# Kernel optimization log

Hardware: AMD Instinct MI355X
Metric: run time of the kernel (lower is better)

The kernel has to match this reference:

```python
import jax, jax.numpy as jnp
import numpy as np

B, L, H, R = 8, 128, 768, 24


def setup_inputs() -> dict:
    key = jax.random.key(0)
    ks = jax.random.split(key, 12)
    s = 0.02  # init scale
    f32 = jnp.float32
    inp = {
        "embed_tokens": jax.random.normal(ks[0], (B, L, H), f32),
        "attention_mask": jnp.ones((B, L), f32),
        "target_rel": jax.random.randint(ks[1], (B,), 0, R),
        # relation-judgement head
        "W_hr": jax.random.normal(ks[2], (H, H // 2), f32) * s,
        "b_hr": jnp.zeros((H // 2,), f32),
        "W_rj": jax.random.normal(ks[3], (H // 2, R), f32) * s,
        "b_rj": jnp.zeros((R,), f32),
        # relation embedding
        "rel_emb": jax.random.normal(ks[4], (R, H), f32) * s,
        # correspondence matrix head (input is concat -> 2H)
        "W_corr": jax.random.normal(ks[5], (2 * H, H), f32) * s,
        "b_corr": jnp.zeros((H,), f32),
        "W_gc": jax.random.normal(ks[6], (H, 1), f32) * s,
        "b_gc": jnp.zeros((1,), f32),
        # subject tagging head (fusion_type='concat' -> 2H in, H hidden)
        "W_sh": jax.random.normal(ks[7], (2 * H, H), f32) * s,
        "b_sh": jnp.zeros((H,), f32),
        "W_st": jax.random.normal(ks[8], (H, 3), f32) * s,
        "b_st": jnp.zeros((3,), f32),
        # object tagging head
        "W_oh": jax.random.normal(ks[9], (2 * H, H), f32) * s,
        "b_oh": jnp.zeros((H,), f32),
        "W_ot": jax.random.normal(ks[10], (H, 3), f32) * s,
        "b_ot": jnp.zeros((3,), f32),
    }
    return inp


def reference(embed_tokens, attention_mask, target_rel,
              W_hr, b_hr, W_rj, b_rj, rel_emb,
              W_corr, b_corr, W_gc, b_gc,
              W_sh, b_sh, W_st, b_st,
              W_oh, b_oh, W_ot, b_ot):
    # ---- stage 1: masked mean-pool + relation judgement (dropout = identity at inference)
    masked = embed_tokens * attention_mask[:, :, None]            # [B,L,H]
    pool = jnp.sum(masked, axis=1) / jnp.sum(attention_mask, axis=1)[:, None]  # [B,H]
    rel_hidden = jax.nn.relu(pool @ W_hr + b_hr)                  # [B,H/2]
    stage1 = rel_hidden @ W_rj + b_rj                             # [B,R]

    # ---- correspondence matrix: concat[b,i,j] = [embed[b,j], embed[b,i]]
    # Decompose concat-linear: concat @ W_corr = embed_j @ W1 + embed_i @ W2
    W1, W2 = W_corr[:H_dim(embed_tokens)], W_corr[H_dim(embed_tokens):]
    A = embed_tokens @ W1                                         # [B,L,H] (j-index part)
    C = embed_tokens @ W2                                         # [B,L,H] (i-index part)
    corres_hidden = jax.nn.relu(A[:, None, :, :] + C[:, :, None, :] + b_corr)  # [B,L,L,H]
    pred_corres = corres_hidden @ W_gc + b_gc                     # [B,L,L,1]

    # ---- relation-fused tagging (mode == 'train')
    re = rel_emb[target_rel]                                      # [B,H]
    Bsz, Lsz, Hsz = embed_tokens.shape
    fusion = jnp.concatenate(
        [jnp.broadcast_to(re[:, None, :], (Bsz, Lsz, Hsz)), embed_tokens], axis=-1)  # [B,L,2H]
    subj = jax.nn.relu(fusion @ W_sh + b_sh) @ W_st + b_st        # [B,L,3]
    obj = jax.nn.relu(fusion @ W_oh + b_oh) @ W_ot + b_ot         # [B,L,3]

    return stage1, subj, obj, pred_corres


def H_dim(x):
    return x.shape[-1]
```

## Files before the change

### kernel.cpp

```cpp
#include <hip/hip_runtime.h>
#include <hip/hip_bf16.h>

#define BD   8
#define LD   128
#define HD   768
#define RD   24
#define H2D  384
#define NF   1536

typedef __attribute__((ext_vector_type(8))) short bf16x8;
typedef __attribute__((ext_vector_type(4))) float f32x4;

__device__ __forceinline__ short f2bf(float f) {
    __hip_bfloat16 h = __float2bfloat16(f);
    return *reinterpret_cast<short*>(&h);
}

__global__ __launch_bounds__(256) void prep_kernel(
        const float* __restrict__ embed, const float* __restrict__ mask,
        const float* __restrict__ rel_emb, const int* __restrict__ trel,
        const float* __restrict__ W_sh, const float* __restrict__ b_sh,
        const float* __restrict__ W_oh, const float* __restrict__ b_oh,
        const float* __restrict__ b_st, const float* __restrict__ b_ot,
        float* __restrict__ pool, float* __restrict__ biasrel,
        float* __restrict__ out_subj, float* __restrict__ out_obj) {
    const int b = blockIdx.x, c = blockIdx.y, tid = threadIdx.x;
    if (c < 12) {
        __shared__ float mrow[LD];
        __shared__ float msum;
        __shared__ float part[4][64];
        if (tid < LD) mrow[tid] = mask[b * LD + tid];
        __syncthreads();
        if (tid == 0) {
            float s = 0.f;
            for (int l = 0; l < LD; ++l) s += mrow[l];
            msum = s;
        }
        __syncthreads();
        const int lc = tid >> 6, hh = tid & 63;
        const int h = c * 64 + hh;
        float acc = 0.f;
        const float* base = embed + ((size_t)b * LD + lc * 32) * HD + h;
#pragma unroll 8
        for (int i = 0; i < 32; ++i) acc += base[(size_t)i * HD] * mrow[lc * 32 + i];
        part[lc][hh] = acc;
        __syncthreads();
        if (lc == 0)
            pool[b * HD + h] = (part[0][hh] + part[1][hh] + part[2][hh] + part[3][hh]) / msum;
    } else {
        const int cc = c - 12;
        __shared__ float re[HD];
        __shared__ float part2[2][128];
        const int rel = trel[b];
        for (int k = tid; k < HD; k += 256) re[k] = rel_emb[(size_t)rel * HD + k];
        if (cc == 0 && tid < 3 * LD) {
            const int l = tid / 3, t = tid - 3 * l;
            out_subj[(b * LD + l) * 3 + t] = b_st[t];
            out_obj [(b * LD + l) * 3 + t] = b_ot[t];
        }
        __syncthreads();
        const int kc = tid >> 7, nn = tid & 127;
        const int n = cc * 128 + nn;
        const float* Wp; float bb; int col;
        if (n < HD) { Wp = W_sh; bb = b_sh[n];      col = n; }
        else        { Wp = W_oh; bb = b_oh[n - HD]; col = n - HD; }
        float acc = 0.f;
#pragma unroll 8
        for (int i = 0; i < 384; ++i) {
            const int k = kc * 384 + i;
            acc += re[k] * Wp[(size_t)k * HD + col];
        }
        part2[kc][nn] = acc;
        __syncthreads();
        if (kc == 0) biasrel[b * NF + n] = part2[0][nn] + part2[1][nn] + bb;
    }
}

__global__ __launch_bounds__(256) void biggemm(
        const float* __restrict__ embed,
        const float* __restrict__ W_corr,
        const float* __restrict__ W_shbot, const float* __restrict__ W_ohbot,
        const float* __restrict__ biasrel,
        const float* __restrict__ W_st, const float* __restrict__ W_ot,
        const float* __restrict__ pool,
        const float* __restrict__ W_hr, const float* __restrict__ b_hr,
        float* __restrict__ AC, float* __restrict__ out_subj,
        float* __restrict__ out_obj, float* __restrict__ rh) {
    const int tid = threadIdx.x;

    if (blockIdx.x >= 24) {
        const int b = blockIdx.y >> 1;
        const int c = (blockIdx.x - 24) * 2 + (blockIdx.y & 1);
        __shared__ float prow[HD];
        __shared__ float rpart[4][64];
        for (int k = tid; k < HD; k += 256) prow[k] = pool[b * HD + k];
        __syncthreads();
        const int kc = tid >> 6, nn = tid & 63;
        const int n = c * 64 + nn;
        float acc = 0.f;
#pragma unroll 8
        for (int i = 0; i < 192; ++i) {
            const int k = kc * 192 + i;
            acc += prow[k] * W_hr[(size_t)k * H2D + n];
        }
        rpart[kc][nn] = acc;
        __syncthreads();
        if (kc == 0)
            rh[b * H2D + n] = fmaxf(rpart[0][nn] + rpart[1][nn] + rpart[2][nn] + rpart[3][nn] + b_hr[n], 0.f);
        return;
    }

    __shared__ __align__(16) short As [64][40];
    __shared__ __align__(16) short Bs0[64][40];
    __shared__ __align__(16) short Bs1[64][40];
    __shared__ float partial[64][3];

    const int bn0 = blockIdx.x * 64;
    const int bm0 = blockIdx.y * 64;

    const float* Wc = (bn0 < HD) ? W_corr  : W_corr + (size_t)HD * HD;
    const float* Wh = (bn0 < HD) ? W_shbot : W_ohbot;
    const int col0 = (bn0 < HD) ? bn0 : bn0 - HD;

    if (tid < 192) partial[tid / 3][tid % 3] = 0.f;

    const int am = tid >> 2;
    const int ak = (tid & 3) * 4;
    const int bn = tid & 63;
    const int bk = (tid >> 6) * 8;

    const int lane = tid & 63;
    const int wv = tid >> 6;
    const int wm = (wv >> 1) * 32;
    const int wn = (wv & 1) * 32;
    const int fr = lane & 15;
    const int kq = (lane >> 4) * 8;
    const int mq = (lane >> 4) * 4;

    f32x4 c00 = {0.f,0.f,0.f,0.f}, c01 = c00, c10 = c00, c11 = c00;
    f32x4 h00 = c00, h01 = c00, h10 = c00, h11 = c00;

    for (int kt = 0; kt < 24; ++kt) {
        const int k0 = kt << 5;
        const float* arow = embed + (size_t)(bm0 + am) * HD + k0;
        float4 va0 = *(const float4*)(arow + ak);
        float4 va1 = *(const float4*)(arow + ak + 16);
        float vb0[8], vb1[8];
#pragma unroll
        for (int j = 0; j < 8; ++j) {
            const size_t widx = (size_t)(k0 + bk + j) * HD + col0 + bn;
            vb0[j] = Wc[widx];
            vb1[j] = Wh[widx];
        }

        __syncthreads();
        {
            short4 s0 = { f2bf(va0.x), f2bf(va0.y), f2bf(va0.z), f2bf(va0.w) };
            short4 s1 = { f2bf(va1.x), f2bf(va1.y), f2bf(va1.z), f2bf(va1.w) };
            *(short4*)&As[am][ak]      = s0;
            *(short4*)&As[am][ak + 16] = s1;
            bf16x8 p0, p1;
#pragma unroll
            for (int j = 0; j < 8; ++j) { p0[j] = f2bf(vb0[j]); p1[j] = f2bf(vb1[j]); }
            *(bf16x8*)&Bs0[bn][bk] = p0;
            *(bf16x8*)&Bs1[bn][bk] = p1;
        }
        __syncthreads();

        bf16x8 a0 = *(bf16x8*)&As[wm + fr][kq];
        bf16x8 a1 = *(bf16x8*)&As[wm + 16 + fr][kq];
        bf16x8 b0 = *(bf16x8*)&Bs0[wn + fr][kq];
        bf16x8 b1 = *(bf16x8*)&Bs0[wn + 16 + fr][kq];
        bf16x8 d0 = *(bf16x8*)&Bs1[wn + fr][kq];
        bf16x8 d1 = *(bf16x8*)&Bs1[wn + 16 + fr][kq];
        c00 = __builtin_amdgcn_mfma_f32_16x16x32_bf16(a0, b0, c00, 0, 0, 0);
        c01 = __builtin_amdgcn_mfma_f32_16x16x32_bf16(a0, b1, c01, 0, 0, 0);
        c10 = __builtin_amdgcn_mfma_f32_16x16x32_bf16(a1, b0, c10, 0, 0, 0);
        c11 = __builtin_amdgcn_mfma_f32_16x16x32_bf16(a1, b1, c11, 0, 0, 0);
        h00 = __builtin_amdgcn_mfma_f32_16x16x32_bf16(a0, d0, h00, 0, 0, 0);
        h01 = __builtin_amdgcn_mfma_f32_16x16x32_bf16(a0, d1, h01, 0, 0, 0);
        h10 = __builtin_amdgcn_mfma_f32_16x16x32_bf16(a1, d0, h10, 0, 0, 0);
        h11 = __builtin_amdgcn_mfma_f32_16x16x32_bf16(a1, d1, h11, 0, 0, 0);
    }

#pragma unroll
    for (int i = 0; i < 2; ++i) {
#pragma unroll
        for (int j = 0; j < 2; ++j) {
            f32x4 a = (i == 0) ? (j == 0 ? c00 : c01) : (j == 0 ? c10 : c11);
            const int ncol = bn0 + wn + j * 16 + fr;
#pragma unroll
            for (int r = 0; r < 4; ++r) {
                const int mrow = bm0 + wm + i * 16 + mq + r;
                AC[(size_t)mrow * NF + ncol] = a[r];
            }
        }
    }

    {
        const float* brl = biasrel + (size_t)(bm0 / LD) * NF;
        const float* Wt = (bn0 < HD) ? W_st : W_ot;
        float* op = (bn0 < HD) ? out_subj : out_obj;
        float pt[8][3] = {};
#pragma unroll
        for (int j = 0; j < 2; ++j) {
            const int ncol = bn0 + wn + j * 16 + fr;
            const int ncl = (bn0 < HD) ? ncol : ncol - HD;
            const float wt0 = Wt[ncl * 3 + 0];
            const float wt1 = Wt[ncl * 3 + 1];
            const float wt2 = Wt[ncl * 3 + 2];
            const float bias = brl[ncol];
#pragma unroll
            for (int i = 0; i < 2; ++i) {
                f32x4 a = (i == 0) ? (j == 0 ? h00 : h01) : (j == 0 ? h10 : h11);
#pragma unroll
                for (int r = 0; r < 4; ++r) {
                    const float v = fmaxf(a[r] + bias, 0.f);
                    pt[i * 4 + r][0] += v * wt0;
                    pt[i * 4 + r][1] += v * wt1;
                    pt[i * 4 + r][2] += v * wt2;
                }
            }
        }
#pragma unroll
        for (int mask = 1; mask < 16; mask <<= 1) {
#pragma unroll
            for (int x = 0; x < 8; ++x)
#pragma unroll
                for (int t = 0; t < 3; ++t)
                    pt[x][t] += __shfl_xor(pt[x][t], mask, 64);
        }
        if (fr == 0) {
#pragma unroll
            for (int i = 0; i < 2; ++i)
#pragma unroll
                for (int r = 0; r < 4; ++r)
#pragma unroll
                    for (int t = 0; t < 3; ++t)
                        atomicAdd(&partial[wm + i * 16 + mq + r][t], pt[i * 4 + r][t]);
        }
        __syncthreads();
        if (tid < 192) {
            const int m = tid / 3, t = tid % 3;
            atomicAdd(&op[(size_t)(bm0 + m) * 3 + t], partial[m][t]);
        }
    }
}

__global__ void corres_kernel(const float* __restrict__ AC,
                              const float* __restrict__ b_corr, const float* __restrict__ W_gc,
                              const float* __restrict__ b_gc,
                              const float* __restrict__ rh,
                              const float* __restrict__ W_rj, const float* __restrict__ b_rj,
                              float* __restrict__ out, float* __restrict__ out_stage1) {
    const int b = blockIdx.y;
    const int tid = threadIdx.x;

    if (blockIdx.x == 32) {
        __shared__ float rl[H2D];
        __shared__ float spart[8][RD];
        for (int k = tid; k < H2D; k += 256) rl[k] = rh[b * H2D + k];
        __syncthreads();
        if (tid < 8 * RD) {
            const int n = tid % RD, kc = tid / RD;
            float acc = 0.f;
#pragma unroll 8
            for (int i = 0; i < 48; ++i) {
                const int k = kc * 48 + i;
                acc += rl[k] * W_rj[k * RD + n];
            }
            spart[kc][n] = acc;
        }
        __syncthreads();
        if (tid < RD) {
            float s = b_rj[tid];
#pragma unroll
            for (int q = 0; q < 8; ++q) s += spart[q][tid];
            out_stage1[b * RD + tid] = s;
        }
        return;
    }

    const int i0 = blockIdx.x * 4;
    const int lane = tid & 63;
    const int wave = tid >> 6;

    float wg[12], cb[4][12];
#pragma unroll
    for (int s = 0; s < 12; ++s) {
        const int h = lane + 64 * s;
        wg[s] = W_gc[h];
        const float bc = b_corr[h];
#pragma unroll
        for (int i = 0; i < 4; ++i)
            cb[i][s] = AC[((size_t)(b * LD + i0 + i)) * NF + HD + h] + bc;
    }
    const float bg = b_gc[0];

    for (int j = wave; j < LD; j += 4) {
        const float* arow = AC + ((size_t)(b * LD + j)) * NF;
        float a[12];
#pragma unroll
        for (int s = 0; s < 12; ++s) a[s] = arow[lane + 64 * s];
        float sum[4] = {0.f, 0.f, 0.f, 0.f};
#pragma unroll
        for (int s = 0; s < 12; ++s) {
#pragma unroll
            for (int i = 0; i < 4; ++i)
                sum[i] += fmaxf(a[s] + cb[i][s], 0.f) * wg[s];
        }
#pragma unroll
        for (int off = 32; off > 0; off >>= 1) {
#pragma unroll
            for (int i = 0; i < 4; ++i) sum[i] += __shfl_down(sum[i], off, 64);
        }
        if (lane == 0) {
#pragma unroll
            for (int i = 0; i < 4; ++i)
                out[((size_t)(b * LD + i0 + i)) * LD + j] = sum[i] + bg;
        }
    }
}

extern "C" void kernel_launch(void* const* d_in, const int* in_sizes, int n_in,
                              void* d_out, int out_size, void* d_ws, size_t ws_size,
                              hipStream_t stream) {
    const float* embed   = (const float*)d_in[0];
    const float* mask    = (const float*)d_in[1];
    const int*   trel    = (const int*)d_in[2];
    const float* W_hr    = (const float*)d_in[3];
    const float* b_hr    = (const float*)d_in[4];
    const float* W_rj    = (const float*)d_in[5];
    const float* b_rj    = (const float*)d_in[6];
    const float* rel_emb = (const float*)d_in[7];
    const float* W_corr  = (const float*)d_in[8];
    const float* b_corr  = (const float*)d_in[9];
    const float* W_gc    = (const float*)d_in[10];
    const float* b_gc    = (const float*)d_in[11];
    const float* W_sh    = (const float*)d_in[12];
    const float* b_sh    = (const float*)d_in[13];
    const float* W_st    = (const float*)d_in[14];
    const float* b_st    = (const float*)d_in[15];
    const float* W_oh    = (const float*)d_in[16];
    const float* b_oh    = (const float*)d_in[17];
    const float* W_ot    = (const float*)d_in[18];
    const float* b_ot    = (const float*)d_in[19];
    float* out = (float*)d_out;

    float* ws      = (float*)d_ws;
    float* AC      = ws;
    float* biasrel = ws + 1572864;
    float* rh      = ws + 1572864 + 12288;
    float* pool    = ws + 1572864 + 12288 + 3072;

    float* out_stage1 = out;
    float* out_subj   = out + 192;
    float* out_obj    = out + 3264;
    float* out_corr   = out + 6336;

    prep_kernel<<<dim3(BD, 24), 256, 0, stream>>>(embed, mask, rel_emb, trel,
                                                  W_sh, b_sh, W_oh, b_oh, b_st, b_ot,
                                                  pool, biasrel, out_subj, out_obj);

    biggemm<<<dim3(27, 16), 256, 0, stream>>>(embed, W_corr,
                                              W_sh + (size_t)HD * HD, W_oh + (size_t)HD * HD,
                                              biasrel, W_st, W_ot, pool, W_hr, b_hr,
                                              AC, out_subj, out_obj, rh);

    corres_kernel<<<dim3(33, BD), 256, 0, stream>>>(AC, b_corr, W_gc, b_gc,
                                                    rh, W_rj, b_rj, out_corr, out_stage1);
}
```

Before: 174.8 us.

## Pre-convert GEMM operands to transposed bf16 and widen corres kernel

```diff
diff --git a/kernel.cpp b/kernel.cpp
--- a/kernel.cpp
+++ b/kernel.cpp
@@ -7,6 +7,7 @@
 #define RD   24
 #define H2D  384
 #define NF   1536
+#define WSZ  589824
 
 typedef __attribute__((ext_vector_type(8))) short bf16x8;
 typedef __attribute__((ext_vector_type(4))) float f32x4;
@@ -19,13 +20,17 @@
 __global__ __launch_bounds__(256) void prep_kernel(
         const float* __restrict__ embed, const float* __restrict__ mask,
         const float* __restrict__ rel_emb, const int* __restrict__ trel,
+        const float* __restrict__ W_corr,
         const float* __restrict__ W_sh, const float* __restrict__ b_sh,
         const float* __restrict__ W_oh, const float* __restrict__ b_oh,
         const float* __restrict__ b_st, const float* __restrict__ b_ot,
         float* __restrict__ pool, float* __restrict__ biasrel,
+        unsigned short* __restrict__ embedB, unsigned short* __restrict__ WT,
         float* __restrict__ out_subj, float* __restrict__ out_obj) {
-    const int b = blockIdx.x, c = blockIdx.y, tid = threadIdx.x;
-    if (c < 12) {
+    const int q = blockIdx.x, tid = threadIdx.x;
+
+    if (q < 96) {
+        const int b = q / 12, c = q % 12;
         __shared__ float mrow[LD];
         __shared__ float msum;
         __shared__ float part[4][64];
@@ -47,13 +52,19 @@
         __syncthreads();
         if (lc == 0)
             pool[b * HD + h] = (part[0][hh] + part[1][hh] + part[2][hh] + part[3][hh]) / msum;
-    } else {
-        const int cc = c - 12;
+    } else if (q < 192) {
+        const int qq = q - 96;
+        const int b = qq / 12, cc = qq % 12;
         __shared__ float re[HD];
         __shared__ float part2[2][128];
         const int rel = trel[b];
         for (int k = tid; k < HD; k += 256) re[k] = rel_emb[(size_t)rel * HD + k];
-        if (cc == 0 && tid < 3 * LD) {
+        if (qq == 0 && tid < 3 * LD) {
+            const int l = tid / 3, t = tid - 3 * l;
+            out_subj[(l) * 3 + t] = b_st[t];
+            out_obj [(l) * 3 + t] = b_ot[t];
+        }
+        if (cc == 0 && b > 0 && tid < 3 * LD) {
             const int l = tid / 3, t = tid - 3 * l;
             out_subj[(b * LD + l) * 3 + t] = b_st[t];
             out_obj [(b * LD + l) * 3 + t] = b_ot[t];
@@ -73,13 +84,53 @@
         part2[kc][nn] = acc;
         __syncthreads();
         if (kc == 0) biasrel[b * NF + n] = part2[0][nn] + part2[1][nn] + bb;
+    } else if (q < 288) {
+        const int base = (q - 192) * 8192;
+#pragma unroll
+        for (int it = 0; it < 4; ++it) {
+            const int off = base + it * 2048 + tid * 8;
+            float4 v0 = *(const float4*)&embed[off];
+            float4 v1 = *(const float4*)&embed[off + 4];
+            bf16x8 p;
+            p[0] = f2bf(v0.x); p[1] = f2bf(v0.y); p[2] = f2bf(v0.z); p[3] = f2bf(v0.w);
+            p[4] = f2bf(v1.x); p[5] = f2bf(v1.y); p[6] = f2bf(v1.z); p[7] = f2bf(v1.w);
+            *(bf16x8*)&embedB[off] = p;
+        }
+    } else {
+        const int qq = q - 288;
+        const int w = qq / 144, t = qq % 144;
+        const int kt = t / 12, nt = t % 12;
+        const float* src = (w == 0) ? W_corr
+                         : (w == 1) ? W_corr + WSZ
+                         : (w == 2) ? W_sh + WSZ
+                                    : W_oh + WSZ;
+        unsigned short* dst = WT + (size_t)w * WSZ;
+        __shared__ float tile[64 * 65];
+        const int r = tid >> 2, c4 = (tid & 3) * 16;
+#pragma unroll
+        for (int i = 0; i < 4; ++i) {
+            float4 v = *(const float4*)&src[(size_t)(kt * 64 + r) * HD + nt * 64 + c4 + i * 4];
+            tile[r * 65 + c4 + i * 4 + 0] = v.x;
+            tile[r * 65 + c4 + i * 4 + 1] = v.y;
+            tile[r * 65 + c4 + i * 4 + 2] = v.z;
+            tile[r * 65 + c4 + i * 4 + 3] = v.w;
+        }
+        __syncthreads();
+        bf16x8 p0, p1;
+#pragma unroll
+        for (int j = 0; j < 8; ++j) {
+            p0[j] = f2bf(tile[(c4 + j) * 65 + r]);
+            p1[j] = f2bf(tile[(c4 + 8 + j) * 65 + r]);
+        }
+        unsigned short* o = dst + (size_t)(nt * 64 + r) * HD + kt * 64 + c4;
+        *(bf16x8*)(o)     = p0;
+        *(bf16x8*)(o + 8) = p1;
     }
 }
 
 __global__ __launch_bounds__(256) void biggemm(
-        const float* __restrict__ embed,
-        const float* __restrict__ W_corr,
-        const float* __restrict__ W_shbot, const float* __restrict__ W_ohbot,
+        const unsigned short* __restrict__ embedB,
+        const unsigned short* __restrict__ WT,
         const float* __restrict__ biasrel,
         const float* __restrict__ W_st, const float* __restrict__ W_ot,
         const float* __restrict__ pool,
@@ -118,16 +169,14 @@
     const int bn0 = blockIdx.x * 64;
     const int bm0 = blockIdx.y * 64;
 
-    const float* Wc = (bn0 < HD) ? W_corr  : W_corr + (size_t)HD * HD;
-    const float* Wh = (bn0 < HD) ? W_shbot : W_ohbot;
+    const unsigned short* W0 = (bn0 < HD) ? WT : WT + WSZ;
+    const unsigned short* W1 = (bn0 < HD) ? WT + 2 * (size_t)WSZ : WT + 3 * (size_t)WSZ;
     const int col0 = (bn0 < HD) ? bn0 : bn0 - HD;
 
     if (tid < 192) partial[tid / 3][tid % 3] = 0.f;
 
-    const int am = tid >> 2;
-    const int ak = (tid & 3) * 4;
-    const int bn = tid & 63;
-    const int bk = (tid >> 6) * 8;
+    const int row = tid >> 2;
+    const int kc8 = (tid & 3) * 8;
 
     const int lane = tid & 63;
     const int wv = tid >> 6;
@@ -142,29 +191,14 @@
 
     for (int kt = 0; kt < 24; ++kt) {
         const int k0 = kt << 5;
-        const float* arow = embed + (size_t)(bm0 + am) * HD + k0;
-        float4 va0 = *(const float4*)(arow + ak);
-        float4 va1 = *(const float4*)(arow + ak + 16);
-        float vb0[8], vb1[8];
-#pragma unroll
-        for (int j = 0; j < 8; ++j) {
-            const size_t widx = (size_t)(k0 + bk + j) * HD + col0 + bn;
-            vb0[j] = Wc[widx];
-            vb1[j] = Wh[widx];
-        }
-
-        __syncthreads();
-        {
-            short4 s0 = { f2bf(va0.x), f2bf(va0.y), f2bf(va0.z), f2bf(va0.w) };
-            short4 s1 = { f2bf(va1.x), f2bf(va1.y), f2bf(va1.z), f2bf(va1.w) };
-            *(short4*)&As[am][ak]      = s0;
-            *(short4*)&As[am][ak + 16] = s1;
-            bf16x8 p0, p1;
-#pragma unroll
-            for (int j = 0; j < 8; ++j) { p0[j] = f2bf(vb0[j]); p1[j] = f2bf(vb1[j]); }
-            *(bf16x8*)&Bs0[bn][bk] = p0;
-            *(bf16x8*)&Bs1[bn][bk] = p1;
-        }
+        bf16x8 av = *(const bf16x8*)&embedB[(size_t)(bm0 + row) * HD + k0 + kc8];
+        bf16x8 b0v = *(const bf16x8*)&W0[(size_t)(col0 + row) * HD + k0 + kc8];
+        bf16x8 b1v = *(const bf16x8*)&W1[(size_t)(col0 + row) * HD + k0 + kc8];
+
+        __syncthreads();
+        *(bf16x8*)&As [row][kc8] = av;
+        *(bf16x8*)&Bs0[row][kc8] = b0v;
+        *(bf16x8*)&Bs1[row][kc8] = b1v;
         __syncthreads();
 
         bf16x8 a0 = *(bf16x8*)&As[wm + fr][kq];
@@ -247,19 +281,20 @@
     }
 }
 
-__global__ void corres_kernel(const float* __restrict__ AC,
-                              const float* __restrict__ b_corr, const float* __restrict__ W_gc,
-                              const float* __restrict__ b_gc,
-                              const float* __restrict__ rh,
-                              const float* __restrict__ W_rj, const float* __restrict__ b_rj,
-                              float* __restrict__ out, float* __restrict__ out_stage1) {
+__global__ __launch_bounds__(512) void corres_kernel(
+        const float* __restrict__ AC,
+        const float* __restrict__ b_corr, const float* __restrict__ W_gc,
+        const float* __restrict__ b_gc,
+        const float* __restrict__ rh,
+        const float* __restrict__ W_rj, const float* __restrict__ b_rj,
+        float* __restrict__ out, float* __restrict__ out_stage1) {
     const int b = blockIdx.y;
     const int tid = threadIdx.x;
 
     if (blockIdx.x == 32) {
         __shared__ float rl[H2D];
         __shared__ float spart[8][RD];
-        for (int k = tid; k < H2D; k += 256) rl[k] = rh[b * H2D + k];
+        if (tid < H2D) rl[tid] = rh[b * H2D + tid];
         __syncthreads();
         if (tid < 8 * RD) {
             const int n = tid % RD, kc = tid / RD;
@@ -285,29 +320,36 @@
     const int lane = tid & 63;
     const int wave = tid >> 6;
 
-    float wg[12], cb[4][12];
-#pragma unroll
-    for (int s = 0; s < 12; ++s) {
-        const int h = lane + 64 * s;
-        wg[s] = W_gc[h];
-        const float bc = b_corr[h];
-#pragma unroll
-        for (int i = 0; i < 4; ++i)
-            cb[i][s] = AC[((size_t)(b * LD + i0 + i)) * NF + HD + h] + bc;
+    f32x4 wg[3], cb[4][3];
+#pragma unroll
+    for (int s = 0; s < 3; ++s) {
+        const int h = s * 256 + lane * 4;
+        f32x4 w = *(const f32x4*)&W_gc[h];
+        f32x4 bc = *(const f32x4*)&b_corr[h];
+        wg[s] = w;
+#pragma unroll
+        for (int i = 0; i < 4; ++i) {
+            f32x4 cv = *(const f32x4*)&AC[((size_t)(b * LD + i0 + i)) * NF + HD + h];
+            cb[i][s] = cv + bc;
+        }
     }
     const float bg = b_gc[0];
 
-    for (int j = wave; j < LD; j += 4) {
+    for (int j = wave; j < LD; j += 8) {
         const float* arow = AC + ((size_t)(b * LD + j)) * NF;
-        float a[12];
-#pragma unroll
-        for (int s = 0; s < 12; ++s) a[s] = arow[lane + 64 * s];
+        f32x4 a[3];
+#pragma unroll
+        for (int s = 0; s < 3; ++s) a[s] = *(const f32x4*)&arow[s * 256 + lane * 4];
         float sum[4] = {0.f, 0.f, 0.f, 0.f};
 #pragma unroll
-        for (int s = 0; s < 12; ++s) {
-#pragma unroll
-            for (int i = 0; i < 4; ++i)
-                sum[i] += fmaxf(a[s] + cb[i][s], 0.f) * wg[s];
+        for (int s = 0; s < 3; ++s) {
+#pragma unroll
+            for (int i = 0; i < 4; ++i) {
+                f32x4 v = a[s] + cb[i][s];
+#pragma unroll
+                for (int t = 0; t < 4; ++t)
+                    sum[i] += fmaxf(v[t], 0.f) * wg[s][t];
+            }
         }
 #pragma unroll
         for (int off = 32; off > 0; off >>= 1) {
@@ -352,21 +394,23 @@
     float* biasrel = ws + 1572864;
     float* rh      = ws + 1572864 + 12288;
     float* pool    = ws + 1572864 + 12288 + 3072;
+    unsigned short* embedB = (unsigned short*)(ws + 1594368);
+    unsigned short* WT     = (unsigned short*)(ws + 1594368 + 393216);
 
     float* out_stage1 = out;
     float* out_subj   = out + 192;
     float* out_obj    = out + 3264;
     float* out_corr   = out + 6336;
 
-    prep_kernel<<<dim3(BD, 24), 256, 0, stream>>>(embed, mask, rel_emb, trel,
-                                                  W_sh, b_sh, W_oh, b_oh, b_st, b_ot,
-                                                  pool, biasrel, out_subj, out_obj);
-
-    biggemm<<<dim3(27, 16), 256, 0, stream>>>(embed, W_corr,
-                                              W_sh + (size_t)HD * HD, W_oh + (size_t)HD * HD,
-                                              biasrel, W_st, W_ot, pool, W_hr, b_hr,
+    prep_kernel<<<864, 256, 0, stream>>>(embed, mask, rel_emb, trel, W_corr,
+                                         W_sh, b_sh, W_oh, b_oh, b_st, b_ot,
+                                         pool, biasrel, embedB, WT,
+                                         out_subj, out_obj);
+
+    biggemm<<<dim3(27, 16), 256, 0, stream>>>(embedB, WT, biasrel, W_st, W_ot,
+                                              pool, W_hr, b_hr,
                                               AC, out_subj, out_obj, rh);
 
-    corres_kernel<<<dim3(33, BD), 256, 0, stream>>>(AC, b_corr, W_gc, b_gc,
+    corres_kernel<<<dim3(33, BD), 512, 0, stream>>>(AC, b_corr, W_gc, b_gc,
                                                     rh, W_rj, b_rj, out_corr, out_stage1);
 }
```

Result: faster. 161.1 us (-7.9%).
